# Performance work log

Measured on AMD Instinct MI355X. Metric: run time of the kernel, lower is better.

Reference implementation:

```python
import jax, jax.numpy as jnp
import numpy as np

B, S, DIN, DOUT, R, E = 4, 4096, 2048, 2048, 16, 12
MULTIPLIER = 1.0
SCALE = 16.0 / 16.0  # alpha / lora_dim


def setup_inputs() -> dict:
    key = jax.random.key(0)
    k_x, k_g, k_org, k_dn, k_up = jax.random.split(key, 5)
    x = jax.random.normal(k_x, (B, S, DIN), dtype=jnp.float32)
    # router gate over experts (external router output; softmax-normalized)
    gate = jax.nn.softmax(jax.random.normal(k_g, (B, E), dtype=jnp.float32), axis=-1)
    W_org = jax.random.normal(k_org, (DOUT, DIN), dtype=jnp.float32) * (1.0 / np.sqrt(DIN))
    W_down = jax.random.normal(k_dn, (R, DIN), dtype=jnp.float32) * (1.0 / np.sqrt(DIN))
    W_up = jax.random.normal(k_up, (E, DOUT, R), dtype=jnp.float32) * 0.02
    return {"x": x, "gate": gate, "W_org": W_org, "W_down": W_down, "W_up": W_up}


def reference(x, gate, W_org, W_down, W_up):
    # Frozen base linear (no bias)
    org = jnp.einsum('bsi,oi->bso', x, W_org)
    # Shared down-projection to rank R
    lx = jnp.einsum('bsi,ri->bsr', x, W_down)                 # [B,S,R]
    # Gate-weighted combination of expert up-projections
    combined = jnp.einsum('be,eor->bor', gate, W_up)          # [B,DOUT,R]
    # Batched low-rank up-projection (torch bmm(lx, combined^T))
    out = jnp.einsum('bsr,bor->bso', lx, combined)            # [B,S,DOUT]
    return org + out * (MULTIPLIER * SCALE)
```

## Files before the change

### kernel.cpp

```cpp
#include <hip/hip_runtime.h>
#include <cstdint>
#include <cstddef>

#define B_    4
#define S_    4096
#define DIN_  2048
#define DOUT_ 2048
#define R_    16
#define E_    12

typedef __bf16 bf16x8  __attribute__((ext_vector_type(8)));
typedef float  floatx4  __attribute__((ext_vector_type(4)));

__device__ __forceinline__ unsigned int f2bf(float f) {
  unsigned int u = __builtin_bit_cast(unsigned int, f);
  u += 0x7fffu + ((u >> 16) & 1u);
  return u >> 16;
}

__device__ __forceinline__ void async_copy16(const void* g, void* l) {
  __builtin_amdgcn_global_load_lds(
      (const __attribute__((address_space(1))) void*)g,
      (__attribute__((address_space(3))) void*)l,
      16, 0, 0);
}

__global__ __launch_bounds__(256) void cvt_x_kernel(const float* __restrict__ x,
                                                    unsigned short* __restrict__ xb) {
  size_t idx = ((size_t)blockIdx.x * 256 + threadIdx.x) * 8;
  float4 a = *(const float4*)(x + idx);
  float4 b = *(const float4*)(x + idx + 4);
  uint4 o;
  o.x = f2bf(a.x) | (f2bf(a.y) << 16);
  o.y = f2bf(a.z) | (f2bf(a.w) << 16);
  o.z = f2bf(b.x) | (f2bf(b.y) << 16);
  o.w = f2bf(b.z) | (f2bf(b.w) << 16);
  *(uint4*)(xb + idx) = o;
}

__global__ __launch_bounds__(256) void prep_misc_kernel(const float* __restrict__ W_org,
                                                        const float* __restrict__ W_down,
                                                        const float* __restrict__ gate,
                                                        const float* __restrict__ W_up,
                                                        unsigned short* __restrict__ worg,
                                                        unsigned short* __restrict__ wdb,
                                                        unsigned short* __restrict__ cmb) {
  const int bid = blockIdx.x;
  const int tid = threadIdx.x;
  if (bid < 2064) {
    const float* src;
    unsigned short* dst;
    size_t idx;
    if (bid < 2048) { src = W_org;  dst = worg; idx = ((size_t)bid * 256 + tid) * 8; }
    else            { src = W_down; dst = wdb;  idx = ((size_t)(bid - 2048) * 256 + tid) * 8; }
    float4 a = *(const float4*)(src + idx);
    float4 b = *(const float4*)(src + idx + 4);
    uint4 o;
    o.x = f2bf(a.x) | (f2bf(a.y) << 16);
    o.y = f2bf(a.z) | (f2bf(a.w) << 16);
    o.z = f2bf(b.x) | (f2bf(b.y) << 16);
    o.w = f2bf(b.z) | (f2bf(b.w) << 16);
    *(uint4*)(dst + idx) = o;
  } else {
    const int idx = (bid - 2064) * 256 + tid;
    const int b   = idx >> 15;
    const int orr = idx & 32767;
    float s = 0.f;
#pragma unroll
    for (int e = 0; e < E_; ++e)
      s += gate[b * E_ + e] * W_up[(size_t)e * DOUT_ * R_ + orr];
    cmb[idx] = (unsigned short)f2bf(s);
  }
}

__global__ __launch_bounds__(256) void lx_kernel(const unsigned short* __restrict__ xb,
                                                 const unsigned short* __restrict__ wdb,
                                                 unsigned short* __restrict__ lxb) {
  const int tid  = threadIdx.x;
  const int lane = tid & 63;
  const int wave = tid >> 6;
  const int grp  = wave >> 1;
  const int kh   = wave & 1;
  const int q    = lane >> 4;
  const int mrow = lane & 15;
  const int row0 = blockIdx.x * 32 + grp * 16;

  floatx4 acc = {};
  const unsigned short* aptr = xb  + (size_t)(row0 + mrow) * DIN_ + kh * 1024 + q * 8;
  const unsigned short* bptr = wdb + (size_t)mrow * DIN_ + kh * 1024 + q * 8;
#pragma unroll 4
  for (int ks = 0; ks < 32; ++ks) {
    bf16x8 av = *(const bf16x8*)(aptr + ks * 32);
    bf16x8 bv = *(const bf16x8*)(bptr + ks * 32);
    acc = __builtin_amdgcn_mfma_f32_16x16x32_bf16(av, bv, acc, 0, 0, 0);
  }

  __shared__ float red[2][64 * 4];
  if (kh == 1) *(floatx4*)&red[grp][lane * 4] = acc;
  __syncthreads();
  if (kh == 0) {
    floatx4 o = *(const floatx4*)&red[grp][lane * 4];
    acc += o;
#pragma unroll
    for (int rg = 0; rg < 4; ++rg)
      lxb[(size_t)(row0 + q * 4 + rg) * R_ + mrow] = (unsigned short)f2bf(acc[rg]);
  }
}

__global__ __launch_bounds__(512, 2) void gemm256_kernel(const unsigned short* __restrict__ A,
                                                         const unsigned short* __restrict__ Bw,
                                                         const unsigned short* __restrict__ lx,
                                                         const unsigned short* __restrict__ cmb,
                                                         float* __restrict__ C) {
  constexpr int K = DIN_;
  __shared__ __align__(16) unsigned short lds[4 * 16384];
  unsigned short* ldsA0 = lds;
  unsigned short* ldsB0 = lds + 16384;
  unsigned short* ldsA1 = lds + 32768;
  unsigned short* ldsB1 = lds + 49152;

  const int tid  = threadIdx.x;
  const int lane = tid & 63;
  const int wave = tid >> 6;
  const int wm   = wave >> 2;
  const int wn   = wave & 3;
  const int u    = lane & 15;
  const int q    = lane >> 4;

  const int lin = blockIdx.x;
  const int swz = (lin & 7) * 64 + (lin >> 3);
  const int by  = swz >> 3;
  const int bx  = swz & 7;
  const int mBase = by * 256;
  const int nBase = bx * 256;
  const int batch = by >> 4;

  const int aBase = (wm * 128 + u) * 64;
  const int bBase = (wn * 64 + u) * 64;
  const int swzK0 = (q ^ (u & 7)) << 3;
  const int swzK1 = ((4 + q) ^ (u & 7)) << 3;

  floatx4 acc[8][4] = {};
  bf16x8 af[4], bfv[4];

  auto stage = [&](const unsigned short* __restrict__ src, unsigned short* dstBase,
                   int rowBase, int k0) {
#pragma unroll
    for (int j = 0; j < 4; ++j) {
      const int p   = j * 8192 + tid * 16;
      const int row = p >> 7;
      const int sp  = (p >> 4) & 7;
      const int ss  = sp ^ (row & 7);
      async_copy16(src + (size_t)(rowBase + row) * K + k0 + ss * 8,
                   (char*)dstBase + p);
    }
  };

  stage(A,  ldsA0, mBase, 0);
  stage(Bw, ldsB0, nBase, 0);
  asm volatile("s_waitcnt vmcnt(0)" ::: "memory");
  __builtin_amdgcn_s_barrier();

#define PHASE(h, SWZ, bufA, bufB, READB, STAGECODE, VMWAIT)                      \
  {                                                                              \
    _Pragma("unroll")                                                            \
    for (int mf2 = 0; mf2 < 4; ++mf2)                                            \
      af[mf2] = *(const bf16x8*)&bufA[aBase + ((h) * 4 + mf2) * 1024 + (SWZ)];   \
    if (READB) {                                                                 \
      _Pragma("unroll")                                                          \
      for (int nf = 0; nf < 4; ++nf)                                             \
        bfv[nf] = *(const bf16x8*)&bufB[bBase + nf * 1024 + (SWZ)];              \
    }                                                                            \
    STAGECODE;                                                                   \
    __builtin_amdgcn_s_barrier();                                                \
    asm volatile("s_waitcnt lgkmcnt(0)" ::: "memory");                           \
    __builtin_amdgcn_s_setprio(1);                                               \
    _Pragma("unroll")                                                            \
    for (int mf2 = 0; mf2 < 4; ++mf2) {                                          \
      _Pragma("unroll")                                                          \
      for (int nf = 0; nf < 4; ++nf)                                             \
        acc[(h) * 4 + mf2][nf] = __builtin_amdgcn_mfma_f32_16x16x32_bf16(        \
            af[mf2], bfv[nf], acc[(h) * 4 + mf2][nf], 0, 0, 0);                  \
    }                                                                            \
    __builtin_amdgcn_s_setprio(0);                                               \
    VMWAIT;                                                                      \
    __builtin_amdgcn_s_barrier();                                                \
  }

  for (int it = 0; it < 16; ++it) {
    const int kB = it * 128 + 64;
    const int kN = it * 128 + 128;
    const bool more = (it < 15);
    PHASE(0, swzK0, ldsA0, ldsB0, true,  stage(A,  ldsA1, mBase, kB), )
    PHASE(1, swzK0, ldsA0, ldsB0, false, stage(Bw, ldsB1, nBase, kB), )
    PHASE(0, swzK1, ldsA0, ldsB0, true,  , )
    PHASE(1, swzK1, ldsA0, ldsB0, false, ,
          asm volatile("s_waitcnt vmcnt(0)" ::: "memory"))
    PHASE(0, swzK0, ldsA1, ldsB1, true,  if (more) stage(A,  ldsA0, mBase, kN), )
    PHASE(1, swzK0, ldsA1, ldsB1, false, if (more) stage(Bw, ldsB0, nBase, kN), )
    PHASE(0, swzK1, ldsA1, ldsB1, true,  , )
    PHASE(1, swzK1, ldsA1, ldsB1, false, ,
          asm volatile("s_waitcnt vmcnt(0)" ::: "memory"))
  }
#undef PHASE

  {
    bf16x8 z = {};
    bf16x8 la[8], lb[4];
#pragma unroll
    for (int mf = 0; mf < 8; ++mf) {
      const size_t row = (size_t)(mBase + wm * 128 + mf * 16 + u);
      const unsigned short* p = lx + row * R_ + (q & 1) * 8;
      la[mf] = (q < 2) ? *(const bf16x8*)p : z;
    }
#pragma unroll
    for (int nf = 0; nf < 4; ++nf) {
      const size_t brow = (size_t)batch * DOUT_ + nBase + wn * 64 + nf * 16 + u;
      const unsigned short* p = cmb + brow * R_ + (q & 1) * 8;
      lb[nf] = (q < 2) ? *(const bf16x8*)p : z;
    }
#pragma unroll
    for (int mf = 0; mf < 8; ++mf)
#pragma unroll
      for (int nf = 0; nf < 4; ++nf)
        acc[mf][nf] = __builtin_amdgcn_mfma_f32_16x16x32_bf16(la[mf], lb[nf],
                                                              acc[mf][nf], 0, 0, 0);
  }

#pragma unroll
  for (int mf = 0; mf < 8; ++mf) {
    const int grow0 = mBase + wm * 128 + mf * 16 + q * 4;
#pragma unroll
    for (int nf = 0; nf < 4; ++nf) {
      const int gcol = nBase + wn * 64 + nf * 16 + u;
#pragma unroll
      for (int rg = 0; rg < 4; ++rg)
        C[(size_t)(grow0 + rg) * DOUT_ + gcol] = acc[mf][nf][rg];
    }
  }
}

extern "C" void kernel_launch(void* const* d_in, const int* in_sizes, int n_in,
                              void* d_out, int out_size, void* d_ws, size_t ws_size,
                              hipStream_t stream) {
  const float* x      = (const float*)d_in[0];
  const float* gate   = (const float*)d_in[1];
  const float* W_org  = (const float*)d_in[2];
  const float* W_down = (const float*)d_in[3];
  const float* W_up   = (const float*)d_in[4];
  float* out = (float*)d_out;

  unsigned short* xb   = (unsigned short*)d_ws;
  unsigned short* worg = xb   + (size_t)B_ * S_ * DIN_;
  unsigned short* wdb  = worg + (size_t)DOUT_ * DIN_;
  unsigned short* lxb  = wdb  + (size_t)R_ * DIN_;
  unsigned short* cmb  = lxb  + (size_t)B_ * S_ * R_;

  cvt_x_kernel<<<(B_ * S_ * DIN_) / 2048, 256, 0, stream>>>(x, xb);

  prep_misc_kernel<<<2576, 256, 0, stream>>>(W_org, W_down, gate, W_up, worg, wdb, cmb);

  lx_kernel<<<(B_ * S_) / 32, 256, 0, stream>>>(xb, wdb, lxb);

  gemm256_kernel<<<512, 512, 0, stream>>>(xb, worg, lxb, cmb, out);
}
```

Measured before the change: 372.3 us.

## Fuse x conversion into down-projection and software-pipeline LDS reads in GEMM

```diff
diff --git a/kernel.cpp b/kernel.cpp
--- a/kernel.cpp
+++ b/kernel.cpp
@@ -23,19 +23,6 @@
       (const __attribute__((address_space(1))) void*)g,
       (__attribute__((address_space(3))) void*)l,
       16, 0, 0);
-}
-
-__global__ __launch_bounds__(256) void cvt_x_kernel(const float* __restrict__ x,
-                                                    unsigned short* __restrict__ xb) {
-  size_t idx = ((size_t)blockIdx.x * 256 + threadIdx.x) * 8;
-  float4 a = *(const float4*)(x + idx);
-  float4 b = *(const float4*)(x + idx + 4);
-  uint4 o;
-  o.x = f2bf(a.x) | (f2bf(a.y) << 16);
-  o.y = f2bf(a.z) | (f2bf(a.w) << 16);
-  o.z = f2bf(b.x) | (f2bf(b.y) << 16);
-  o.w = f2bf(b.z) | (f2bf(b.w) << 16);
-  *(uint4*)(xb + idx) = o;
 }
 
 __global__ __launch_bounds__(256) void prep_misc_kernel(const float* __restrict__ W_org,
@@ -73,9 +60,10 @@
   }
 }
 
-__global__ __launch_bounds__(256) void lx_kernel(const unsigned short* __restrict__ xb,
-                                                 const unsigned short* __restrict__ wdb,
-                                                 unsigned short* __restrict__ lxb) {
+__global__ __launch_bounds__(256) void lx_fused_kernel(const float* __restrict__ x,
+                                                       const unsigned short* __restrict__ wdb,
+                                                       unsigned short* __restrict__ xb,
+                                                       unsigned short* __restrict__ lxb) {
   const int tid  = threadIdx.x;
   const int lane = tid & 63;
   const int wave = tid >> 6;
@@ -86,11 +74,21 @@
   const int row0 = blockIdx.x * 32 + grp * 16;
 
   floatx4 acc = {};
-  const unsigned short* aptr = xb  + (size_t)(row0 + mrow) * DIN_ + kh * 1024 + q * 8;
+  const size_t rowOff = (size_t)(row0 + mrow) * DIN_ + kh * 1024 + q * 8;
+  const float* aptr = x + rowOff;
+  unsigned short* xbp = xb + rowOff;
   const unsigned short* bptr = wdb + (size_t)mrow * DIN_ + kh * 1024 + q * 8;
 #pragma unroll 4
   for (int ks = 0; ks < 32; ++ks) {
-    bf16x8 av = *(const bf16x8*)(aptr + ks * 32);
+    float4 a0 = *(const float4*)(aptr + ks * 32);
+    float4 a1 = *(const float4*)(aptr + ks * 32 + 4);
+    uint4 o;
+    o.x = f2bf(a0.x) | (f2bf(a0.y) << 16);
+    o.y = f2bf(a0.z) | (f2bf(a0.w) << 16);
+    o.z = f2bf(a1.x) | (f2bf(a1.y) << 16);
+    o.w = f2bf(a1.z) | (f2bf(a1.w) << 16);
+    *(uint4*)(xbp + ks * 32) = o;
+    bf16x8 av = __builtin_bit_cast(bf16x8, o);
     bf16x8 bv = *(const bf16x8*)(bptr + ks * 32);
     acc = __builtin_amdgcn_mfma_f32_16x16x32_bf16(av, bv, acc, 0, 0, 0);
   }
@@ -99,8 +97,8 @@
   if (kh == 1) *(floatx4*)&red[grp][lane * 4] = acc;
   __syncthreads();
   if (kh == 0) {
-    floatx4 o = *(const floatx4*)&red[grp][lane * 4];
-    acc += o;
+    floatx4 o2 = *(const floatx4*)&red[grp][lane * 4];
+    acc += o2;
 #pragma unroll
     for (int rg = 0; rg < 4; ++rg)
       lxb[(size_t)(row0 + q * 4 + rg) * R_ + mrow] = (unsigned short)f2bf(acc[rg]);
@@ -141,7 +139,8 @@
   const int swzK1 = ((4 + q) ^ (u & 7)) << 3;
 
   floatx4 acc[8][4] = {};
-  bf16x8 af[4], bfv[4];
+  bf16x8 afb[2][4];
+  bf16x8 bfb[2][4];
 
   auto stage = [&](const unsigned short* __restrict__ src, unsigned short* dstBase,
                    int rowBase, int k0) {
@@ -156,53 +155,77 @@
     }
   };
 
-  stage(A,  ldsA0, mBase, 0);
-  stage(Bw, ldsB0, nBase, 0);
-  asm volatile("s_waitcnt vmcnt(0)" ::: "memory");
-  __builtin_amdgcn_s_barrier();
-
-#define PHASE(h, SWZ, bufA, bufB, READB, STAGECODE, VMWAIT)                      \
+#define RDA(dst, bufA, h, SWZ)                                                   \
   {                                                                              \
     _Pragma("unroll")                                                            \
     for (int mf2 = 0; mf2 < 4; ++mf2)                                            \
-      af[mf2] = *(const bf16x8*)&bufA[aBase + ((h) * 4 + mf2) * 1024 + (SWZ)];   \
-    if (READB) {                                                                 \
-      _Pragma("unroll")                                                          \
-      for (int nf = 0; nf < 4; ++nf)                                             \
-        bfv[nf] = *(const bf16x8*)&bufB[bBase + nf * 1024 + (SWZ)];              \
-    }                                                                            \
-    STAGECODE;                                                                   \
-    __builtin_amdgcn_s_barrier();                                                \
-    asm volatile("s_waitcnt lgkmcnt(0)" ::: "memory");                           \
+      afb[dst][mf2] = *(const bf16x8*)&bufA[aBase + ((h) * 4 + mf2) * 1024 + (SWZ)]; \
+  }
+#define RDB(dst, bufB, SWZ)                                                      \
+  {                                                                              \
+    _Pragma("unroll")                                                            \
+    for (int nf = 0; nf < 4; ++nf)                                               \
+      bfb[dst][nf] = *(const bf16x8*)&bufB[bBase + nf * 1024 + (SWZ)];           \
+  }
+#define MM(h, bp)                                                                \
+  {                                                                              \
+    __builtin_amdgcn_sched_barrier(0);                                           \
     __builtin_amdgcn_s_setprio(1);                                               \
     _Pragma("unroll")                                                            \
     for (int mf2 = 0; mf2 < 4; ++mf2) {                                          \
       _Pragma("unroll")                                                          \
       for (int nf = 0; nf < 4; ++nf)                                             \
         acc[(h) * 4 + mf2][nf] = __builtin_amdgcn_mfma_f32_16x16x32_bf16(        \
-            af[mf2], bfv[nf], acc[(h) * 4 + mf2][nf], 0, 0, 0);                  \
+            afb[(h)][mf2], bfb[(bp)][nf], acc[(h) * 4 + mf2][nf], 0, 0, 0);      \
     }                                                                            \
     __builtin_amdgcn_s_setprio(0);                                               \
-    VMWAIT;                                                                      \
-    __builtin_amdgcn_s_barrier();                                                \
-  }
+  }
+#define BAR()                                                                    \
+  __builtin_amdgcn_s_barrier();                                                  \
+  __builtin_amdgcn_sched_barrier(0);
+
+  stage(A,  ldsA0, mBase, 0);
+  stage(Bw, ldsB0, nBase, 0);
+  asm volatile("s_waitcnt vmcnt(0)" ::: "memory");
+  BAR();
+  RDA(0, ldsA0, 0, swzK0);
+  RDB(0, ldsB0, swzK0);
 
   for (int it = 0; it < 16; ++it) {
     const int kB = it * 128 + 64;
     const int kN = it * 128 + 128;
     const bool more = (it < 15);
-    PHASE(0, swzK0, ldsA0, ldsB0, true,  stage(A,  ldsA1, mBase, kB), )
-    PHASE(1, swzK0, ldsA0, ldsB0, false, stage(Bw, ldsB1, nBase, kB), )
-    PHASE(0, swzK1, ldsA0, ldsB0, true,  , )
-    PHASE(1, swzK1, ldsA0, ldsB0, false, ,
-          asm volatile("s_waitcnt vmcnt(0)" ::: "memory"))
-    PHASE(0, swzK0, ldsA1, ldsB1, true,  if (more) stage(A,  ldsA0, mBase, kN), )
-    PHASE(1, swzK0, ldsA1, ldsB1, false, if (more) stage(Bw, ldsB0, nBase, kN), )
-    PHASE(0, swzK1, ldsA1, ldsB1, true,  , )
-    PHASE(1, swzK1, ldsA1, ldsB1, false, ,
-          asm volatile("s_waitcnt vmcnt(0)" ::: "memory"))
-  }
-#undef PHASE
+    stage(A,  ldsA1, mBase, kB);
+    stage(Bw, ldsB1, nBase, kB);
+    RDA(1, ldsA0, 1, swzK0);
+    MM(0, 0); BAR();
+    RDA(0, ldsA0, 0, swzK1);
+    RDB(1, ldsB0, swzK1);
+    MM(1, 0); BAR();
+    RDA(1, ldsA0, 1, swzK1);
+    MM(0, 1);
+    asm volatile("s_waitcnt vmcnt(0)" ::: "memory");
+    BAR();
+    RDA(0, ldsA1, 0, swzK0);
+    RDB(0, ldsB1, swzK0);
+    MM(1, 1); BAR();
+    if (more) { stage(A, ldsA0, mBase, kN); stage(Bw, ldsB0, nBase, kN); }
+    RDA(1, ldsA1, 1, swzK0);
+    MM(0, 0); BAR();
+    RDA(0, ldsA1, 0, swzK1);
+    RDB(1, ldsB1, swzK1);
+    MM(1, 0); BAR();
+    RDA(1, ldsA1, 1, swzK1);
+    MM(0, 1);
+    asm volatile("s_waitcnt vmcnt(0)" ::: "memory");
+    BAR();
+    if (more) { RDA(0, ldsA0, 0, swzK0); RDB(0, ldsB0, swzK0); }
+    MM(1, 1); BAR();
+  }
+#undef RDA
+#undef RDB
+#undef MM
+#undef BAR
 
   {
     bf16x8 z = {};
@@ -235,7 +258,8 @@
       const int gcol = nBase + wn * 64 + nf * 16 + u;
 #pragma unroll
       for (int rg = 0; rg < 4; ++rg)
-        C[(size_t)(grow0 + rg) * DOUT_ + gcol] = acc[mf][nf][rg];
+        __builtin_nontemporal_store(acc[mf][nf][rg],
+                                    &C[(size_t)(grow0 + rg) * DOUT_ + gcol]);
     }
   }
 }
@@ -256,11 +280,9 @@
   unsigned short* lxb  = wdb  + (size_t)R_ * DIN_;
   unsigned short* cmb  = lxb  + (size_t)B_ * S_ * R_;
 
-  cvt_x_kernel<<<(B_ * S_ * DIN_) / 2048, 256, 0, stream>>>(x, xb);
-
   prep_misc_kernel<<<2576, 256, 0, stream>>>(W_org, W_down, gate, W_up, worg, wdb, cmb);
 
-  lx_kernel<<<(B_ * S_) / 32, 256, 0, stream>>>(xb, wdb, lxb);
+  lx_fused_kernel<<<(B_ * S_) / 32, 256, 0, stream>>>(x, wdb, xb, lxb);
 
   gemm256_kernel<<<512, 512, 0, stream>>>(xb, worg, lxb, cmb, out);
 }
```

After: 389.8 us. 1.05x slower.

## Prefetch a full K-block ahead with partial vmcnt waits in GEMM main loop

Applied to the files above, without the earlier changes.

```diff
diff --git a/kernel.cpp b/kernel.cpp
--- a/kernel.cpp
+++ b/kernel.cpp
@@ -156,24 +156,19 @@
     }
   };
 
-  stage(A,  ldsA0, mBase, 0);
-  stage(Bw, ldsB0, nBase, 0);
-  asm volatile("s_waitcnt vmcnt(0)" ::: "memory");
-  __builtin_amdgcn_s_barrier();
-
-#define PHASE(h, SWZ, bufA, bufB, READB, STAGECODE, VMWAIT)                      \
+#define PHASE(h, bufA_, bufB_, READB, SWZ, STAGECODE, VMWAIT)                    \
   {                                                                              \
     _Pragma("unroll")                                                            \
     for (int mf2 = 0; mf2 < 4; ++mf2)                                            \
-      af[mf2] = *(const bf16x8*)&bufA[aBase + ((h) * 4 + mf2) * 1024 + (SWZ)];   \
+      af[mf2] = *(const bf16x8*)&bufA_[aBase + ((h) * 4 + mf2) * 1024 + (SWZ)];  \
     if (READB) {                                                                 \
       _Pragma("unroll")                                                          \
       for (int nf = 0; nf < 4; ++nf)                                             \
-        bfv[nf] = *(const bf16x8*)&bufB[bBase + nf * 1024 + (SWZ)];              \
+        bfv[nf] = *(const bf16x8*)&bufB_[bBase + nf * 1024 + (SWZ)];             \
     }                                                                            \
-    STAGECODE;                                                                   \
     __builtin_amdgcn_s_barrier();                                                \
     asm volatile("s_waitcnt lgkmcnt(0)" ::: "memory");                           \
+    STAGECODE;                                                                   \
     __builtin_amdgcn_s_setprio(1);                                               \
     _Pragma("unroll")                                                            \
     for (int mf2 = 0; mf2 < 4; ++mf2) {                                          \
@@ -187,20 +182,30 @@
     __builtin_amdgcn_s_barrier();                                                \
   }
 
+  stage(A,  ldsA0, mBase, 0);
+  stage(Bw, ldsB0, nBase, 0);
+  stage(A,  ldsA1, mBase, 64);
+  stage(Bw, ldsB1, nBase, 64);
+  asm volatile("s_waitcnt vmcnt(8)" ::: "memory");
+  __builtin_amdgcn_s_barrier();
+
   for (int it = 0; it < 16; ++it) {
-    const int kB = it * 128 + 64;
-    const int kN = it * 128 + 128;
+    const int kN0 = it * 128 + 128;
+    const int kN1 = it * 128 + 192;
     const bool more = (it < 15);
-    PHASE(0, swzK0, ldsA0, ldsB0, true,  stage(A,  ldsA1, mBase, kB), )
-    PHASE(1, swzK0, ldsA0, ldsB0, false, stage(Bw, ldsB1, nBase, kB), )
-    PHASE(0, swzK1, ldsA0, ldsB0, true,  , )
-    PHASE(1, swzK1, ldsA0, ldsB0, false, ,
-          asm volatile("s_waitcnt vmcnt(0)" ::: "memory"))
-    PHASE(0, swzK0, ldsA1, ldsB1, true,  if (more) stage(A,  ldsA0, mBase, kN), )
-    PHASE(1, swzK0, ldsA1, ldsB1, false, if (more) stage(Bw, ldsB0, nBase, kN), )
-    PHASE(0, swzK1, ldsA1, ldsB1, true,  , )
-    PHASE(1, swzK1, ldsA1, ldsB1, false, ,
-          asm volatile("s_waitcnt vmcnt(0)" ::: "memory"))
+    PHASE(0, ldsA0, ldsB0, true,  swzK0, , )
+    PHASE(1, ldsA0, ldsB0, false, swzK0, , )
+    PHASE(0, ldsA0, ldsB0, true,  swzK1, , )
+    PHASE(1, ldsA0, ldsB0, false, swzK1,
+          if (more) { stage(A, ldsA0, mBase, kN0); stage(Bw, ldsB0, nBase, kN0); },
+          if (more) { asm volatile("s_waitcnt vmcnt(8)" ::: "memory"); }
+          else      { asm volatile("s_waitcnt vmcnt(0)" ::: "memory"); })
+    PHASE(0, ldsA1, ldsB1, true,  swzK0, , )
+    PHASE(1, ldsA1, ldsB1, false, swzK0, , )
+    PHASE(0, ldsA1, ldsB1, true,  swzK1, , )
+    PHASE(1, ldsA1, ldsB1, false, swzK1,
+          if (more) { stage(A, ldsA1, mBase, kN1); stage(Bw, ldsB1, nBase, kN1); },
+          if (more) { asm volatile("s_waitcnt vmcnt(8)" ::: "memory"); })
   }
 #undef PHASE
 
```

Result: no change. 376.3 us (+1.1%).
